# Optimization experiments

Hardware: AMD Instinct MI355X
Metric: run time of the kernel (lower is better)

The kernel has to match this reference:

```python
import jax, jax.numpy as jnp
import numpy as np

B, N_IN, NV, F = 1, 65536, 1, 64
N_OUT, K = 16384, 16
N_DIST, N_PHI, OUT = 4, 8, 256
DIST_MAX = 0.1  # grid_layers[level_out].min_dist stand-in


def setup_inputs() -> dict:
    key = jax.random.key(0)
    ks = jax.random.split(key, 6)
    x = jax.random.normal(ks[0], (B, N_IN, NV, F), dtype=jnp.float32)
    nh_idx = jax.random.randint(ks[1], (N_OUT, K), 0, N_IN)  # neighbor gather indices
    d_dists = jax.random.uniform(ks[2], (N_OUT, K), dtype=jnp.float32) * DIST_MAX
    d_phi = jax.random.uniform(ks[3], (N_OUT, K), dtype=jnp.float32) * (2 * np.pi) - np.pi
    dists = jnp.linspace(0.0, DIST_MAX, N_DIST, dtype=jnp.float32)          # anchor distances
    sigma = jnp.asarray(DIST_MAX / 2, dtype=jnp.float32)                     # n_sigma == 1 -> scalar
    phi = jnp.linspace(-np.pi, np.pi, N_PHI + 1, dtype=jnp.float32)[:-1]     # von Mises: phi_min = -pi
    kappa = jnp.asarray(1.0, dtype=jnp.float32)                              # kappa_init
    W_out = jax.random.normal(ks[4], (F * N_DIST * N_PHI, OUT), dtype=jnp.float32) / np.sqrt(F * N_DIST * N_PHI)
    return {"x": x, "d_dists": d_dists, "d_phi": d_phi, "dists": dists,
            "sigma": sigma, "kappa": kappa, "phi": phi, "W_out": W_out, "nh_idx": nh_idx}


def reference(x, d_dists, d_phi, dists, sigma, kappa, phi, W_out, nh_idx):
    # Gaussian distance kernel: exp(-0.5*((d - dist_k)/sigma)^2)  -> (N_OUT, K, N_DIST)
    w_d = jnp.exp(-0.5 * ((d_dists[..., None] - dists) / sigma) ** 2)
    # von Mises angular kernel: exp(kappa * cos(d_phi - phi_p))   -> (N_OUT, K, N_PHI)
    w_p = jnp.exp(kappa * jnp.cos(d_phi[..., None] - phi))
    # combined kernel weights, normalized over the K neighbors per anchor
    w = w_d[..., :, None] * w_p[..., None, :]                      # (N_OUT, K, N_DIST, N_PHI)
    w = w / (jnp.sum(w, axis=1, keepdims=True) + 1e-9)
    w = w.reshape(N_OUT, K, N_DIST * N_PHI)                        # (N_OUT, K, M)
    # gather neighbor features from the input grid
    x_nb = x[:, nh_idx]                                            # (B, N_OUT, K, NV, F)
    # weighted aggregation over neighbors -> enhanced channels
    agg = jnp.einsum('bnkvf,nkm->bnvmf', x_nb, w)                  # (B, N_OUT, NV, M, F)
    agg = agg.reshape(B, N_OUT, NV, N_DIST * N_PHI * F)            # model_dim_enhanced = 2048
    return agg @ W_out                                             # (B, N_OUT, NV, OUT)
```

## Files before the change

kernel.cpp:

```cpp
#include <hip/hip_runtime.h>
#include <hip/hip_bf16.h>

#define N_IN   65536
#define N_OUTP 16384
#define KNB    16
#define FDIM   64
#define M_DIM  32
#define KDIM   2048
#define OUT_D  256

typedef __bf16 bf16x8_t __attribute__((ext_vector_type(8)));
typedef float  f32x4_t  __attribute__((ext_vector_type(4)));
typedef float  f32x2_t  __attribute__((ext_vector_type(2)));


__device__ __forceinline__ unsigned pk2(float a, float b) {
  __bf16 b0 = (__bf16)a, b1 = (__bf16)b;
  return ((unsigned)__builtin_bit_cast(unsigned short, b1) << 16) |
          (unsigned)__builtin_bit_cast(unsigned short, b0);
}

__global__ __launch_bounds__(256) void pack_B_kernel(
    const float* __restrict__ W, uint4* __restrict__ Bws)
{
  __shared__ float wlds[32 * 260];
  const int kk = blockIdx.x;
  const int t  = threadIdx.x;

  const float4* Wb = (const float4*)(W + kk * 32 * OUT_D);
#pragma unroll
  for (int i = 0; i < 8; ++i) {
    int idx = i * 256 + t;
    int row = idx >> 6, c4 = idx & 63;
    float4 v = Wb[idx];
    *(float4*)(wlds + row * 260 + c4 * 4) = v;
  }
  __syncthreads();

#pragma unroll
  for (int j = 0; j < 4; ++j) {
    int c  = j * 256 + t;
    int l  = c & 63, nt = c >> 6;
    int r0 = (l >> 4) * 8, col = nt * 16 + (l & 15);
    union { unsigned short s[8]; uint4 v; } u;
#pragma unroll
    for (int jj = 0; jj < 8; ++jj) {
      __bf16 b = (__bf16)wlds[(r0 + jj) * 260 + col];
      u.s[jj] = __builtin_bit_cast(unsigned short, b);
    }
    Bws[(size_t)kk * 1024 + c] = u.v;
  }
}

#define WST 580
#define WKS 36
#define XPS 576
#define XPK 36

__global__ __launch_bounds__(256, 4) void agg_kernel(
    const float* __restrict__ x,
    const float* __restrict__ d_dists,
    const float* __restrict__ d_phi,
    const float* __restrict__ dists,
    const float* __restrict__ sigma_p,
    const float* __restrict__ kappa_p,
    const float* __restrict__ phi,
    const int*   __restrict__ nh_idx,
    uint4*       __restrict__ Aws)
{
  __shared__ __align__(16) float    wbuf[8 * WST];
  __shared__ __align__(16) unsigned xpk[8 * XPS];

  const int t  = threadIdx.x;
  const int n0 = blockIdx.x * 8;
  const int T  = blockIdx.x >> 1;
  const int r0 = (blockIdx.x & 1) * 8;

  const int h = t & 1, gk = (t >> 1) & 15, gr8 = t >> 5;
  const int gidx = nh_idx[(n0 + gr8) * KNB + gk];
  const float4* xr = (const float4*)x + (size_t)gidx * 16 + h * 8;
  float4 xreg[8];
#pragma unroll
  for (int j = 0; j < 8; ++j) xreg[j] = xr[j];

  {
    const float sinv = 1.0f / sigma_p[0];
    const float kap  = kappa_p[0];
    float phiv[8], distv[4];
#pragma unroll
    for (int p = 0; p < 8; ++p) phiv[p] = phi[p];
#pragma unroll
    for (int d = 0; d < 4; ++d) distv[d] = dists[d];

    int rk = t >> 1, r8w = rk >> 4, k = rk & 15, rep = t & 1;
    int n = n0 + r8w;
    float dd = d_dists[n * KNB + k];
    float dp = d_phi[n * KNB + k];
    float wp[8];
#pragma unroll
    for (int p = 0; p < 8; ++p) wp[p] = __expf(kap * __cosf(dp - phiv[p]));
#pragma unroll
    for (int dl = 0; dl < 2; ++dl) {
      int d = rep * 2 + dl;
      float td = (dd - distv[d]) * sinv;
      float wd = __expf(-0.5f * td * td);
      float* dst = wbuf + r8w * WST + k * WKS + d * 8;
      *(float4*)(dst)     = make_float4(wd * wp[0], wd * wp[1], wd * wp[2], wd * wp[3]);
      *(float4*)(dst + 4) = make_float4(wd * wp[4], wd * wp[5], wd * wp[6], wd * wp[7]);
    }
  }

  {
    unsigned u[16];
#pragma unroll
    for (int j = 0; j < 8; ++j) {
      u[2 * j]     = pk2(xreg[j].x, xreg[j].y);
      u[2 * j + 1] = pk2(xreg[j].z, xreg[j].w);
    }
    uint4* xd = (uint4*)(xpk + gr8 * XPS + gk * XPK + h * 16);
#pragma unroll
    for (int q = 0; q < 4; ++q)
      xd[q] = make_uint4(u[4 * q], u[4 * q + 1], u[4 * q + 2], u[4 * q + 3]);
  }
  __syncthreads();

  {
    int nr8 = t >> 5, m = t & 31;
    float wv[16];
    float s = 0.f;
#pragma unroll
    for (int k = 0; k < 16; ++k) {
      wv[k] = wbuf[nr8 * WST + k * WKS + m];
      s += wv[k];
    }
    float wn = 1.0f / (s + 1e-9f);
#pragma unroll
    for (int k = 0; k < 16; ++k)
      wbuf[nr8 * WST + k * WKS + m] = wv[k] * wn;
  }
  __syncthreads();

  {
    const int r8 = t & 7, fo = (t >> 3) & 7, mq = t >> 6;
    f32x2_t acc[8][4];
#pragma unroll
    for (int mi = 0; mi < 8; ++mi)
#pragma unroll
      for (int fj = 0; fj < 4; ++fj) acc[mi][fj] = (f32x2_t){0.f, 0.f};

    const float*    wp_ = wbuf + r8 * WST + mq * 8;
    const unsigned* xp_ = xpk + r8 * XPS + fo * 4;

#pragma unroll 8
    for (int k = 0; k < 16; ++k) {
      uint4 xu = *(const uint4*)(xp_ + k * XPK);
      float4 wa = *(const float4*)(wp_ + k * WKS);
      float4 wb = *(const float4*)(wp_ + k * WKS + 4);
      float wv[8] = {wa.x, wa.y, wa.z, wa.w, wb.x, wb.y, wb.z, wb.w};
      f32x2_t xv[4];
      xv[0] = (f32x2_t){__builtin_bit_cast(float, xu.x << 16),
                        __builtin_bit_cast(float, xu.x & 0xffff0000u)};
      xv[1] = (f32x2_t){__builtin_bit_cast(float, xu.y << 16),
                        __builtin_bit_cast(float, xu.y & 0xffff0000u)};
      xv[2] = (f32x2_t){__builtin_bit_cast(float, xu.z << 16),
                        __builtin_bit_cast(float, xu.z & 0xffff0000u)};
      xv[3] = (f32x2_t){__builtin_bit_cast(float, xu.w << 16),
                        __builtin_bit_cast(float, xu.w & 0xffff0000u)};
#pragma unroll
      for (int mi = 0; mi < 8; ++mi) {
        f32x2_t wm = (f32x2_t){wv[mi], wv[mi]};
#pragma unroll
        for (int fj = 0; fj < 4; ++fj)
          acc[mi][fj] += wm * xv[fj];
      }
    }

    uint4* base = Aws + (size_t)T * 4096 + (fo & 3) * 16 + r0 + r8
                      + (size_t)(fo >> 2) * 64;
#pragma unroll
    for (int mi = 0; mi < 8; ++mi) {
      int m = mq * 8 + mi;
      uint4 v;
      v.x = pk2(acc[mi][0][0], acc[mi][0][1]);
      v.y = pk2(acc[mi][1][0], acc[mi][1][1]);
      v.z = pk2(acc[mi][2][0], acc[mi][2][1]);
      v.w = pk2(acc[mi][3][0], acc[mi][3][1]);
      base[m * 128] = v;
    }
  }
}

__global__ __launch_bounds__(512, 2) void gemm_kernel(
    const uint4* __restrict__ Astream,
    const uint4* __restrict__ Bws,
    float*       __restrict__ out)
{
  __shared__ float red[4][64 * 68];

  const int t    = threadIdx.x;
  const int lane = t & 63;
  const int w    = t >> 6;
  const int cg   = w & 3;
  const int half = w >> 2;
  const int rb   = blockIdx.x;

  const uint4* pa = Astream + (size_t)(rb * 4) * 4096 + half * 64 + lane;
  const uint4* pb = Bws + (half * 16 + cg * 4) * 64 + lane;

  f32x4_t cacc[4][4];
#pragma unroll
  for (int mt = 0; mt < 4; ++mt)
#pragma unroll
    for (int i = 0; i < 4; ++i)
      cacc[mt][i] = (f32x4_t){0.f, 0.f, 0.f, 0.f};

  uint4 a[4][4], b[4][4];
#pragma unroll
  for (int s = 0; s < 4; ++s) {
#pragma unroll
    for (int mt = 0; mt < 4; ++mt) a[s][mt] = pa[mt * 4096 + s * 128];
#pragma unroll
    for (int i = 0; i < 4; ++i)    b[s][i]  = pb[s * 2048 + i * 64];
  }

#pragma unroll 4
  for (int j = 0; j < 32; ++j) {
    const int s = j & 3;
    bf16x8_t B0 = __builtin_bit_cast(bf16x8_t, b[s][0]);
    bf16x8_t B1 = __builtin_bit_cast(bf16x8_t, b[s][1]);
    bf16x8_t B2 = __builtin_bit_cast(bf16x8_t, b[s][2]);
    bf16x8_t B3 = __builtin_bit_cast(bf16x8_t, b[s][3]);
#pragma unroll
    for (int mt = 0; mt < 4; ++mt) {
      bf16x8_t A = __builtin_bit_cast(bf16x8_t, a[s][mt]);
      cacc[mt][0] = __builtin_amdgcn_mfma_f32_16x16x32_bf16(A, B0, cacc[mt][0], 0, 0, 0);
      cacc[mt][1] = __builtin_amdgcn_mfma_f32_16x16x32_bf16(A, B1, cacc[mt][1], 0, 0, 0);
      cacc[mt][2] = __builtin_amdgcn_mfma_f32_16x16x32_bf16(A, B2, cacc[mt][2], 0, 0, 0);
      cacc[mt][3] = __builtin_amdgcn_mfma_f32_16x16x32_bf16(A, B3, cacc[mt][3], 0, 0, 0);
    }
    if (j < 28) {
#pragma unroll
      for (int mt = 0; mt < 4; ++mt) a[s][mt] = pa[mt * 4096 + (j + 4) * 128];
#pragma unroll
      for (int i = 0; i < 4; ++i)    b[s][i]  = pb[(j + 4) * 2048 + i * 64];
    }
  }

  const int lrow = (lane >> 4) * 4;
  const int lcol = lane & 15;

  if (half == 0) {
#pragma unroll
    for (int mt = 0; mt < 4; ++mt)
#pragma unroll
      for (int i = 0; i < 4; ++i)
#pragma unroll
        for (int reg = 0; reg < 4; ++reg)
          red[cg][(mt * 16 + lrow + reg) * 68 + i * 16 + lcol] = cacc[mt][i][reg];
  }
  __syncthreads();
  if (half == 1) {
#pragma unroll
    for (int mt = 0; mt < 4; ++mt)
#pragma unroll
      for (int i = 0; i < 4; ++i)
#pragma unroll
        for (int reg = 0; reg < 4; ++reg) {
          int row = mt * 16 + lrow + reg;
          int col = i * 16 + lcol;
          float v = red[cg][row * 68 + col] + cacc[mt][i][reg];
          out[(rb * 64 + row) * OUT_D + cg * 64 + col] = v;
        }
  }
}

extern "C" void kernel_launch(void* const* d_in, const int* in_sizes, int n_in,
                              void* d_out, int out_size, void* d_ws, size_t ws_size,
                              hipStream_t stream) {
  const float* x      = (const float*)d_in[0];
  const float* dd     = (const float*)d_in[1];
  const float* dp     = (const float*)d_in[2];
  const float* dists  = (const float*)d_in[3];
  const float* sigma  = (const float*)d_in[4];
  const float* kappa  = (const float*)d_in[5];
  const float* phi    = (const float*)d_in[6];
  const float* W      = (const float*)d_in[7];
  const int*   nh     = (const int*)d_in[8];
  float*       out    = (float*)d_out;

  uint4* Bws = (uint4*)d_ws;
  uint4* Aws = (uint4*)((char*)d_ws + (1 << 20));

  pack_B_kernel<<<64, 256, 0, stream>>>(W, Bws);
  agg_kernel<<<N_OUTP / 8, 256, 0, stream>>>(
      x, dd, dp, dists, sigma, kappa, phi, nh, Aws);
  gemm_kernel<<<N_OUTP / 64, 512, 0, stream>>>(Aws, Bws, out);
}
```

Measured before the change: 58.62 us.

## Store neighbor weights as bf16 in LDS, swizzle block order, raise occupancy

The per-neighbor kernel weights are now packed as bf16 pairs in shared memory instead of fp32, which roughly halves that buffer and the LDS traffic. Normalization runs on 128 threads, each handling two packed columns, and the launch bound asks for 5 blocks per CU instead of 4. Block indices are also remapped with an 8x8 swizzle inside groups of 64, changing the order in which output tiles are written. Rounding the weights to bf16 before normalizing and again after adds precision loss, and the tighter launch bound may constrain registers.

```diff
diff --git a/kernel.cpp b/kernel.cpp
--- a/kernel.cpp
+++ b/kernel.cpp
@@ -19,6 +19,12 @@
   return ((unsigned)__builtin_bit_cast(unsigned short, b1) << 16) |
           (unsigned)__builtin_bit_cast(unsigned short, b0);
 }
+__device__ __forceinline__ float ulo(unsigned u) {
+  return __builtin_bit_cast(float, u << 16);
+}
+__device__ __forceinline__ float uhi(unsigned u) {
+  return __builtin_bit_cast(float, u & 0xffff0000u);
+}
 
 __global__ __launch_bounds__(256) void pack_B_kernel(
     const float* __restrict__ W, uint4* __restrict__ Bws)
@@ -52,12 +58,12 @@
   }
 }
 
-#define WST 580
-#define WKS 36
-#define XPS 576
-#define XPK 36
-
-__global__ __launch_bounds__(256, 4) void agg_kernel(
+#define WBST 324
+#define WBK  20
+#define XPS  576
+#define XPK  36
+
+__global__ __launch_bounds__(256, 5) void agg_kernel(
     const float* __restrict__ x,
     const float* __restrict__ d_dists,
     const float* __restrict__ d_phi,
@@ -68,13 +74,15 @@
     const int*   __restrict__ nh_idx,
     uint4*       __restrict__ Aws)
 {
-  __shared__ __align__(16) float    wbuf[8 * WST];
+  __shared__ __align__(16) unsigned wb[8 * WBST];
   __shared__ __align__(16) unsigned xpk[8 * XPS];
 
-  const int t  = threadIdx.x;
-  const int n0 = blockIdx.x * 8;
-  const int T  = blockIdx.x >> 1;
-  const int r0 = (blockIdx.x & 1) * 8;
+  const int t = threadIdx.x;
+  const int b = blockIdx.x;
+  const int w = (b & ~63) | ((b & 7) << 3) | ((b >> 3) & 7);
+  const int n0 = w * 8;
+  const int T  = w >> 1;
+  const int r0 = (w & 1) * 8;
 
   const int h = t & 1, gk = (t >> 1) & 15, gr8 = t >> 5;
   const int gidx = nh_idx[(n0 + gr8) * KNB + gk];
@@ -99,14 +107,19 @@
     float wp[8];
 #pragma unroll
     for (int p = 0; p < 8; ++p) wp[p] = __expf(kap * __cosf(dp - phiv[p]));
+
+    unsigned* dst = wb + r8w * WBST + k * WBK + rep * 8;
 #pragma unroll
     for (int dl = 0; dl < 2; ++dl) {
       int d = rep * 2 + dl;
       float td = (dd - distv[d]) * sinv;
       float wd = __expf(-0.5f * td * td);
-      float* dst = wbuf + r8w * WST + k * WKS + d * 8;
-      *(float4*)(dst)     = make_float4(wd * wp[0], wd * wp[1], wd * wp[2], wd * wp[3]);
-      *(float4*)(dst + 4) = make_float4(wd * wp[4], wd * wp[5], wd * wp[6], wd * wp[7]);
+      uint4 v;
+      v.x = pk2(wd * wp[0], wd * wp[1]);
+      v.y = pk2(wd * wp[2], wd * wp[3]);
+      v.z = pk2(wd * wp[4], wd * wp[5]);
+      v.w = pk2(wd * wp[6], wd * wp[7]);
+      *(uint4*)(dst + dl * 4) = v;
     }
   }
 
@@ -124,19 +137,22 @@
   }
   __syncthreads();
 
-  {
-    int nr8 = t >> 5, m = t & 31;
-    float wv[16];
-    float s = 0.f;
+  if (t < 128) {
+    int nr8 = t >> 4, mc = t & 15;
+    unsigned* col = wb + nr8 * WBST + mc;
+    unsigned v[16];
+    float s0 = 0.f, s1 = 0.f;
 #pragma unroll
     for (int k = 0; k < 16; ++k) {
-      wv[k] = wbuf[nr8 * WST + k * WKS + m];
-      s += wv[k];
-    }
-    float wn = 1.0f / (s + 1e-9f);
+      v[k] = col[k * WBK];
+      s0 += ulo(v[k]);
+      s1 += uhi(v[k]);
+    }
+    float i0 = 1.0f / (s0 + 1e-9f);
+    float i1 = 1.0f / (s1 + 1e-9f);
 #pragma unroll
     for (int k = 0; k < 16; ++k)
-      wbuf[nr8 * WST + k * WKS + m] = wv[k] * wn;
+      col[k * WBK] = pk2(ulo(v[k]) * i0, uhi(v[k]) * i1);
   }
   __syncthreads();
 
@@ -148,30 +164,26 @@
 #pragma unroll
       for (int fj = 0; fj < 4; ++fj) acc[mi][fj] = (f32x2_t){0.f, 0.f};
 
-    const float*    wp_ = wbuf + r8 * WST + mq * 8;
     const unsigned* xp_ = xpk + r8 * XPS + fo * 4;
+    const unsigned* wp_ = wb + r8 * WBST + mq * 4;
 
 #pragma unroll 8
     for (int k = 0; k < 16; ++k) {
       uint4 xu = *(const uint4*)(xp_ + k * XPK);
-      float4 wa = *(const float4*)(wp_ + k * WKS);
-      float4 wb = *(const float4*)(wp_ + k * WKS + 4);
-      float wv[8] = {wa.x, wa.y, wa.z, wa.w, wb.x, wb.y, wb.z, wb.w};
+      uint4 wu = *(const uint4*)(wp_ + k * WBK);
+      float wm[8] = {ulo(wu.x), uhi(wu.x), ulo(wu.y), uhi(wu.y),
+                     ulo(wu.z), uhi(wu.z), ulo(wu.w), uhi(wu.w)};
       f32x2_t xv[4];
-      xv[0] = (f32x2_t){__builtin_bit_cast(float, xu.x << 16),
-                        __builtin_bit_cast(float, xu.x & 0xffff0000u)};
-      xv[1] = (f32x2_t){__builtin_bit_cast(float, xu.y << 16),
-                        __builtin_bit_cast(float, xu.y & 0xffff0000u)};
-      xv[2] = (f32x2_t){__builtin_bit_cast(float, xu.z << 16),
-                        __builtin_bit_cast(float, xu.z & 0xffff0000u)};
-      xv[3] = (f32x2_t){__builtin_bit_cast(float, xu.w << 16),
-                        __builtin_bit_cast(float, xu.w & 0xffff0000u)};
+      xv[0] = (f32x2_t){ulo(xu.x), uhi(xu.x)};
+      xv[1] = (f32x2_t){ulo(xu.y), uhi(xu.y)};
+      xv[2] = (f32x2_t){ulo(xu.z), uhi(xu.z)};
+      xv[3] = (f32x2_t){ulo(xu.w), uhi(xu.w)};
 #pragma unroll
       for (int mi = 0; mi < 8; ++mi) {
-        f32x2_t wm = (f32x2_t){wv[mi], wv[mi]};
+        f32x2_t wmm = (f32x2_t){wm[mi], wm[mi]};
 #pragma unroll
         for (int fj = 0; fj < 4; ++fj)
-          acc[mi][fj] += wm * xv[fj];
+          acc[mi][fj] += wmm * xv[fj];
       }
     }
 
```

Result: slower. 83.93 us (+43.2%).

## Fold weight packing into agg kernel and defer neighbor normalization to epilogue

Applied to the files above, without the earlier changes.

Removes the separate pack_B launch by having the first 64 agg blocks convert W to bf16 tiles after their main work, reusing the same shared memory buffer. The per-anchor normalization pass over the weight buffer, along with its extra barrier, is replaced by accumulating the weight sums inside the main loop and scaling the accumulators once before the bf16 store. This saves a kernel launch and a shared-memory pass, but adds tail work to 64 blocks and a small amount of extra register pressure.

```diff
diff --git a/kernel.cpp b/kernel.cpp
--- a/kernel.cpp
+++ b/kernel.cpp
@@ -19,43 +19,18 @@
   return ((unsigned)__builtin_bit_cast(unsigned short, b1) << 16) |
           (unsigned)__builtin_bit_cast(unsigned short, b0);
 }
-
-__global__ __launch_bounds__(256) void pack_B_kernel(
-    const float* __restrict__ W, uint4* __restrict__ Bws)
-{
-  __shared__ float wlds[32 * 260];
-  const int kk = blockIdx.x;
-  const int t  = threadIdx.x;
-
-  const float4* Wb = (const float4*)(W + kk * 32 * OUT_D);
-#pragma unroll
-  for (int i = 0; i < 8; ++i) {
-    int idx = i * 256 + t;
-    int row = idx >> 6, c4 = idx & 63;
-    float4 v = Wb[idx];
-    *(float4*)(wlds + row * 260 + c4 * 4) = v;
-  }
-  __syncthreads();
-
-#pragma unroll
-  for (int j = 0; j < 4; ++j) {
-    int c  = j * 256 + t;
-    int l  = c & 63, nt = c >> 6;
-    int r0 = (l >> 4) * 8, col = nt * 16 + (l & 15);
-    union { unsigned short s[8]; uint4 v; } u;
-#pragma unroll
-    for (int jj = 0; jj < 8; ++jj) {
-      __bf16 b = (__bf16)wlds[(r0 + jj) * 260 + col];
-      u.s[jj] = __builtin_bit_cast(unsigned short, b);
-    }
-    Bws[(size_t)kk * 1024 + c] = u.v;
-  }
+__device__ __forceinline__ float ulo(unsigned u) {
+  return __builtin_bit_cast(float, u << 16);
+}
+__device__ __forceinline__ float uhi(unsigned u) {
+  return __builtin_bit_cast(float, u & 0xffff0000u);
 }
 
 #define WST 580
 #define WKS 36
 #define XPS 576
 #define XPK 36
+#define AGG_LDS 36992
 
 __global__ __launch_bounds__(256, 4) void agg_kernel(
     const float* __restrict__ x,
@@ -65,11 +40,14 @@
     const float* __restrict__ sigma_p,
     const float* __restrict__ kappa_p,
     const float* __restrict__ phi,
+    const float* __restrict__ W,
     const int*   __restrict__ nh_idx,
-    uint4*       __restrict__ Aws)
+    uint4*       __restrict__ Aws,
+    uint4*       __restrict__ Bws)
 {
-  __shared__ __align__(16) float    wbuf[8 * WST];
-  __shared__ __align__(16) unsigned xpk[8 * XPS];
+  __shared__ __align__(16) char smem_raw[AGG_LDS];
+  float*    wbuf = (float*)smem_raw;
+  unsigned* xpk  = (unsigned*)(smem_raw + 18560);
 
   const int t  = threadIdx.x;
   const int n0 = blockIdx.x * 8;
@@ -125,53 +103,37 @@
   __syncthreads();
 
   {
-    int nr8 = t >> 5, m = t & 31;
-    float wv[16];
-    float s = 0.f;
-#pragma unroll
-    for (int k = 0; k < 16; ++k) {
-      wv[k] = wbuf[nr8 * WST + k * WKS + m];
-      s += wv[k];
-    }
-    float wn = 1.0f / (s + 1e-9f);
-#pragma unroll
-    for (int k = 0; k < 16; ++k)
-      wbuf[nr8 * WST + k * WKS + m] = wv[k] * wn;
-  }
-  __syncthreads();
-
-  {
     const int r8 = t & 7, fo = (t >> 3) & 7, mq = t >> 6;
     f32x2_t acc[8][4];
-#pragma unroll
-    for (int mi = 0; mi < 8; ++mi)
+    float   den[8];
+#pragma unroll
+    for (int mi = 0; mi < 8; ++mi) {
+      den[mi] = 0.f;
 #pragma unroll
       for (int fj = 0; fj < 4; ++fj) acc[mi][fj] = (f32x2_t){0.f, 0.f};
+    }
 
     const float*    wp_ = wbuf + r8 * WST + mq * 8;
     const unsigned* xp_ = xpk + r8 * XPS + fo * 4;
 
 #pragma unroll 8
     for (int k = 0; k < 16; ++k) {
+      float4 wa = *(const float4*)(wp_ + k * WKS);
+      float4 wbv = *(const float4*)(wp_ + k * WKS + 4);
       uint4 xu = *(const uint4*)(xp_ + k * XPK);
-      float4 wa = *(const float4*)(wp_ + k * WKS);
-      float4 wb = *(const float4*)(wp_ + k * WKS + 4);
-      float wv[8] = {wa.x, wa.y, wa.z, wa.w, wb.x, wb.y, wb.z, wb.w};
+      float wv[8] = {wa.x, wa.y, wa.z, wa.w, wbv.x, wbv.y, wbv.z, wbv.w};
       f32x2_t xv[4];
-      xv[0] = (f32x2_t){__builtin_bit_cast(float, xu.x << 16),
-                        __builtin_bit_cast(float, xu.x & 0xffff0000u)};
-      xv[1] = (f32x2_t){__builtin_bit_cast(float, xu.y << 16),
-                        __builtin_bit_cast(float, xu.y & 0xffff0000u)};
-      xv[2] = (f32x2_t){__builtin_bit_cast(float, xu.z << 16),
-                        __builtin_bit_cast(float, xu.z & 0xffff0000u)};
-      xv[3] = (f32x2_t){__builtin_bit_cast(float, xu.w << 16),
-                        __builtin_bit_cast(float, xu.w & 0xffff0000u)};
+      xv[0] = (f32x2_t){ulo(xu.x), uhi(xu.x)};
+      xv[1] = (f32x2_t){ulo(xu.y), uhi(xu.y)};
+      xv[2] = (f32x2_t){ulo(xu.z), uhi(xu.z)};
+      xv[3] = (f32x2_t){ulo(xu.w), uhi(xu.w)};
 #pragma unroll
       for (int mi = 0; mi < 8; ++mi) {
-        f32x2_t wm = (f32x2_t){wv[mi], wv[mi]};
+        den[mi] += wv[mi];
+        f32x2_t wmm = (f32x2_t){wv[mi], wv[mi]};
 #pragma unroll
         for (int fj = 0; fj < 4; ++fj)
-          acc[mi][fj] += wm * xv[fj];
+          acc[mi][fj] += wmm * xv[fj];
       }
     }
 
@@ -180,12 +142,43 @@
 #pragma unroll
     for (int mi = 0; mi < 8; ++mi) {
       int m = mq * 8 + mi;
+      float wn = 1.0f / (den[mi] + 1e-9f);
       uint4 v;
-      v.x = pk2(acc[mi][0][0], acc[mi][0][1]);
-      v.y = pk2(acc[mi][1][0], acc[mi][1][1]);
-      v.z = pk2(acc[mi][2][0], acc[mi][2][1]);
-      v.w = pk2(acc[mi][3][0], acc[mi][3][1]);
+      v.x = pk2(acc[mi][0][0] * wn, acc[mi][0][1] * wn);
+      v.y = pk2(acc[mi][1][0] * wn, acc[mi][1][1] * wn);
+      v.z = pk2(acc[mi][2][0] * wn, acc[mi][2][1] * wn);
+      v.w = pk2(acc[mi][3][0] * wn, acc[mi][3][1] * wn);
       base[m * 128] = v;
+    }
+  }
+
+  if (blockIdx.x < 64) {
+    __syncthreads();
+    float* wlds = (float*)smem_raw;
+    const int kk = blockIdx.x;
+
+    const float4* Wb = (const float4*)(W + kk * 32 * OUT_D);
+#pragma unroll
+    for (int i = 0; i < 8; ++i) {
+      int idx = i * 256 + t;
+      int row = idx >> 6, c4 = idx & 63;
+      float4 v = Wb[idx];
+      *(float4*)(wlds + row * 260 + c4 * 4) = v;
+    }
+    __syncthreads();
+
+#pragma unroll
+    for (int j = 0; j < 4; ++j) {
+      int c  = j * 256 + t;
+      int l  = c & 63, nt = c >> 6;
+      int rr = (l >> 4) * 8, col = nt * 16 + (l & 15);
+      union { unsigned short s[8]; uint4 v; } u;
+#pragma unroll
+      for (int jj = 0; jj < 8; ++jj) {
+        __bf16 b = (__bf16)wlds[(rr + jj) * 260 + col];
+        u.s[jj] = __builtin_bit_cast(unsigned short, b);
+      }
+      Bws[(size_t)kk * 1024 + c] = u.v;
     }
   }
 }
@@ -291,8 +284,7 @@
   uint4* Bws = (uint4*)d_ws;
   uint4* Aws = (uint4*)((char*)d_ws + (1 << 20));
 
-  pack_B_kernel<<<64, 256, 0, stream>>>(W, Bws);
   agg_kernel<<<N_OUTP / 8, 256, 0, stream>>>(
-      x, dd, dp, dists, sigma, kappa, phi, nh, Aws);
+      x, dd, dp, dists, sigma, kappa, phi, W, nh, Aws, Bws);
   gemm_kernel<<<N_OUTP / 64, 512, 0, stream>>>(Aws, Bws, out);
 }
```

After: 58.10 us, median of 2. About the same (-0.9%).
